# Kernel tuning notes

Hardware: AMD Instinct MI355X
Metric: run time of the kernel (lower is better)

The kernel has to match this reference:

```python
import jax, jax.numpy as jnp
import numpy as np

B, S, D = 2, 2048, 1024
NH, KVH = 16, 4
HD = D // NH  # 64
ROPE_BASE = 10000.0


def rotate_half(x):
    half = x.shape[-1] // 2
    x1, x2 = x[..., :half], x[..., half:]
    return jnp.concatenate((-x2, x1), axis=-1)


def rope_cache(seq_len, head_dim, base, dtype):
    half = head_dim // 2
    inv_freq = 1.0 / (base ** (jnp.arange(half, dtype=jnp.float32) / max(1, half)))
    t = jnp.arange(seq_len, dtype=jnp.float32)
    freqs = jnp.einsum('i,j->ij', t, inv_freq)          # [S, half]
    emb = jnp.concatenate((freqs, freqs), axis=-1)      # [S, HD]
    cos = jnp.cos(emb)[None, None].astype(dtype)        # [1,1,S,HD]
    sin = jnp.sin(emb)[None, None].astype(dtype)
    return sin, cos


def setup_inputs() -> dict:
    key = jax.random.key(0)
    ks = jax.random.split(key, 5)
    s = 0.02
    return {
        'x': jax.random.normal(ks[0], (B, S, D), dtype=jnp.float32),
        'Wq': jax.random.normal(ks[1], (D, D), dtype=jnp.float32) * s,
        'Wk': jax.random.normal(ks[2], (D, KVH * HD), dtype=jnp.float32) * s,
        'Wv': jax.random.normal(ks[3], (D, KVH * HD), dtype=jnp.float32) * s,
        'Wo': jax.random.normal(ks[4], (D, D), dtype=jnp.float32) * s,
    }


def reference(x, Wq, Wk, Wv, Wo):
    bsz, seq_len, _ = x.shape
    scale = HD ** -0.5
    q = (x @ Wq).reshape(bsz, seq_len, NH, HD).transpose(0, 2, 1, 3)   # [B,NH,S,HD]
    k = (x @ Wk).reshape(bsz, seq_len, KVH, HD).transpose(0, 2, 1, 3)  # [B,KVH,S,HD]
    v = (x @ Wv).reshape(bsz, seq_len, KVH, HD).transpose(0, 2, 1, 3)

    sin, cos = rope_cache(seq_len, HD, ROPE_BASE, q.dtype)
    q = q * cos + rotate_half(q) * sin
    k = k * cos + rotate_half(k) * sin

    rep = NH // KVH
    k = jnp.repeat(k, rep, axis=1)  # repeat_interleave over head dim -> [B,NH,S,HD]
    v = jnp.repeat(v, rep, axis=1)

    att = jnp.einsum('bhqd,bhkd->bhqk', q, k) * scale
    causal = jnp.tril(jnp.ones((seq_len, seq_len), dtype=bool))
    att = jnp.where(causal, att, jnp.finfo(att.dtype).min)
    att = jax.nn.softmax(att, axis=-1)

    y = jnp.einsum('bhqk,bhkd->bhqd', att, v)
    y = y.transpose(0, 2, 1, 3).reshape(bsz, seq_len, NH * HD)
    return y @ Wo
```

## Files before the change

### kernel.cpp

```cpp
#include <hip/hip_runtime.h>

typedef __bf16 bf16x8 __attribute__((ext_vector_type(8)));
typedef float  f32x4  __attribute__((ext_vector_type(4)));
typedef float  f32x16 __attribute__((ext_vector_type(16)));
typedef unsigned short u16;
typedef unsigned int u32;
typedef u16 u16x8 __attribute__((ext_vector_type(8)));
typedef u32 u32x4 __attribute__((ext_vector_type(4)));

#define MFMA16(a, b, c) __builtin_amdgcn_mfma_f32_16x16x32_bf16((a), (b), (c), 0, 0, 0)
#define MFMA32(a, b, c) __builtin_amdgcn_mfma_f32_32x32x16_bf16((a), (b), (c), 0, 0, 0)

__device__ __forceinline__ u16 f2bf(float f) {
  __bf16 b = (__bf16)f;
  return __builtin_bit_cast(u16, b);
}
__device__ __forceinline__ bf16x8 ld_bf8(const u16* p) {
  return __builtin_bit_cast(bf16x8, *(const u16x8*)p);
}
__device__ __forceinline__ float ex2(float x) { return __builtin_amdgcn_exp2f(x); }
__device__ __forceinline__ void pswap(u32& a, u32& b) {
  asm("v_permlane32_swap_b32 %0, %1" : "+v"(a), "+v"(b));
}

__global__ __launch_bounds__(256) void k_prep(const float4* __restrict__ x,
                                              ushort4* __restrict__ xb,
                                              const float* __restrict__ Wq,
                                              const float* __restrict__ Wk,
                                              const float* __restrict__ Wv,
                                              const float* __restrict__ Wo,
                                              u16* __restrict__ WqkvT,
                                              u16* __restrict__ WoT,
                                              float2* __restrict__ tab) {
  __shared__ float t[64][65];
  int bid = blockIdx.x;
  if (bid < 4096) {
    int i = bid * 256 + threadIdx.x;
    float4 v = x[i];
    ushort4 o;
    o.x = f2bf(v.x); o.y = f2bf(v.y); o.z = f2bf(v.z); o.w = f2bf(v.w);
    xb[i] = o;
  } else if (bid < 4736) {
    int tb = bid - 4096;
    int n0 = (tb % 40) * 64, k0 = (tb / 40) * 64;
    int c = threadIdx.x & 63, r = threadIdx.x >> 6;
    int n = n0 + c;
    const float* sp; int stride; int nn;
    if (n < 1024)      { sp = Wq; stride = 1024; nn = n; }
    else if (n < 1280) { sp = Wk; stride = 256;  nn = n - 1024; }
    else if (n < 1536) { sp = Wv; stride = 256;  nn = n - 1280; }
    else               { sp = Wo; stride = 1024; nn = n - 1536; }
#pragma unroll
    for (int j = 0; j < 16; ++j)
      t[r + j * 4][c] = sp[(size_t)(k0 + r + j * 4) * stride + nn];
    __syncthreads();
#pragma unroll
    for (int j = 0; j < 16; ++j) {
      int rr = r + j * 4;
      int orow = n0 + rr;
      u16* d = (orow < 1536) ? (WqkvT + (size_t)orow * 1024)
                             : (WoT + (size_t)(orow - 1536) * 1024);
      d[k0 + c] = f2bf(t[c][rr]);
    }
  } else {
    int idx = (bid - 4736) * 256 + threadIdx.x;
    int s = idx >> 5, j = idx & 31;
    const float L2B = 13.287712379549449f / 32.f;
    float ang = (float)s * exp2f(-(float)j * L2B);
    float sn, cs; sincosf(ang, &sn, &cs);
    tab[idx] = make_float2(cs, sn);
  }
}

__global__ __launch_bounds__(256) void k_gemm1(const u16* __restrict__ A,
                                               const u16* __restrict__ Bt,
                                               const float2* __restrict__ tab,
                                               u16* __restrict__ Qa,
                                               u16* __restrict__ Ka,
                                               u16* __restrict__ Vtt) {
  const int K = 1024;
  __shared__ u16 lA[128 * 64];
  __shared__ u16 lB[128 * 64];
  const int t = threadIdx.x;
  const int lane = t & 63;
  const int w = t >> 6;
  const int lg = lane >> 4, lr = lane & 15;
  const int wr = w >> 1, wc = w & 1;
  int f = blockIdx.x;
  int cpx = 384 >> 3;
  int f2 = (f & 7) * cpx + (f >> 3);
  const int n0 = (f2 % 12) * 128, m0 = (f2 / 12) * 128;

  f32x4 acc[4][4];
#pragma unroll
  for (int a = 0; a < 4; ++a)
#pragma unroll
    for (int b = 0; b < 4; ++b) acc[a][b] = (f32x4)0.0f;

  for (int kt = 0; kt < K; kt += 64) {
#pragma unroll
    for (int i = 0; i < 4; ++i) {
      int c = t + i * 256;
      int row = c >> 3, slot = c & 7;
      int k8 = (slot ^ (row & 7)) << 3;
      __builtin_amdgcn_global_load_lds(
          (const __attribute__((address_space(1))) void*)(A + (size_t)(m0 + row) * K + kt + k8),
          (__attribute__((address_space(3))) void*)(&lA[c * 8]), 16, 0, 0);
    }
#pragma unroll
    for (int i = 0; i < 4; ++i) {
      int c = t + i * 256;
      int row = c >> 3, slot = c & 7;
      int k8 = (slot ^ (row & 7)) << 3;
      __builtin_amdgcn_global_load_lds(
          (const __attribute__((address_space(1))) void*)(Bt + (size_t)(n0 + row) * K + kt + k8),
          (__attribute__((address_space(3))) void*)(&lB[c * 8]), 16, 0, 0);
    }
    asm volatile("s_waitcnt vmcnt(0)" ::: "memory");
    __syncthreads();

#pragma unroll
    for (int ks = 0; ks < 2; ++ks) {
      bf16x8 af[4], bff[4];
#pragma unroll
      for (int mf = 0; mf < 4; ++mf) {
        int row = wr * 64 + mf * 16 + lr;
        int eo = (ks * 32 + lg * 8) ^ ((row & 7) << 3);
        af[mf] = ld_bf8(&lA[row * 64 + eo]);
      }
#pragma unroll
      for (int nf = 0; nf < 4; ++nf) {
        int row = wc * 64 + nf * 16 + lr;
        int eo = (ks * 32 + lg * 8) ^ ((row & 7) << 3);
        bff[nf] = ld_bf8(&lB[row * 64 + eo]);
      }
#pragma unroll
      for (int mf = 0; mf < 4; ++mf)
#pragma unroll
        for (int nf = 0; nf < 4; ++nf)
          acc[mf][nf] = MFMA16(af[mf], bff[nf], acc[mf][nf]);
    }
    __syncthreads();
  }

  const int colbase = n0 + wc * 64;
  if (colbase < 1280) {
    const bool isQ = colbase < 1024;
    const float SC = isQ ? 0.18033688f : 1.0f;
    u16* base;
    if (isQ) {
      int hh = colbase >> 6;
      base = Qa + (size_t)hh * 2048 * 64;
    } else {
      int kvh = (colbase - 1024) >> 6;
      base = Ka + (size_t)kvh * 2048 * 64;
    }
    const int hstride = isQ ? 16 : 4;
#pragma unroll
    for (int mf = 0; mf < 4; ++mf)
#pragma unroll
      for (int i2 = 0; i2 < 4; ++i2) {
        int row = m0 + wr * 64 + mf * 16 + lg * 4 + i2;
        int bb = row >> 11, ss = row & 2047;
        float2 t0 = tab[ss * 32 + lr];
        float2 t1 = tab[ss * 32 + 16 + lr];
        float v0 = acc[mf][0][i2], v2 = acc[mf][2][i2];
        float v1 = acc[mf][1][i2], v3 = acc[mf][3][i2];
        u16* dst = base + ((size_t)bb * hstride * 2048 + ss) * 64;
        dst[lr]      = f2bf((v0 * t0.x - v2 * t0.y) * SC);
        dst[lr + 32] = f2bf((v2 * t0.x + v0 * t0.y) * SC);
        dst[lr + 16] = f2bf((v1 * t1.x - v3 * t1.y) * SC);
        dst[lr + 48] = f2bf((v3 * t1.x + v1 * t1.y) * SC);
      }
  } else {
    int kvh = (colbase - 1280) >> 6;
#pragma unroll
    for (int mf = 0; mf < 4; ++mf)
#pragma unroll
      for (int i2 = 0; i2 < 4; ++i2) {
        int row = m0 + wr * 64 + mf * 16 + lg * 4 + i2;
        int bb = row >> 11, ss = row & 2047;
        u16* dst = Vtt + (size_t)(bb * 4 + kvh) * 131072 +
                   (size_t)(ss >> 5) * 2048 + (ss & 31);
#pragma unroll
        for (int nf = 0; nf < 4; ++nf)
          dst[(nf * 16 + lr) * 32] = f2bf(acc[mf][nf][i2]);
      }
  }
}

#define PK2(a, b) ((u32)f2bf(a) | ((u32)f2bf(b) << 16))

#define GLL(SRC, DST) __builtin_amdgcn_global_load_lds(                     \
    (const __attribute__((address_space(1))) void*)(SRC),                   \
    (__attribute__((address_space(3))) void*)(DST), 16, 0, 0)

#define STAGE(DB, J2) do {                                                  \
    GLL(ksrc0 + (size_t)(J2) * 4096,        &kbuf[DB][t * 8]);              \
    GLL(ksrc0 + (size_t)(J2) * 4096 + 2048, &kbuf[DB][2048 + t * 8]);       \
    GLL(vsrc0 + (size_t)(J2) * 4096,        &vbuf[DB][t * 8]);              \
    GLL(vsrc0 + (size_t)(J2) * 4096 + 2048, &vbuf[DB][2048 + t * 8]);       \
  } while (0)

#define SUBC(SOFF, KB, QLIM) do {                                           \
    bf16x8 KF0 = ld_bf8(kb_ + (SOFF) + ql * 64 + (((0 + hi) ^ (ql & 7)) << 3)); \
    bf16x8 KF1 = ld_bf8(kb_ + (SOFF) + ql * 64 + (((2 + hi) ^ (ql & 7)) << 3)); \
    bf16x8 KF2 = ld_bf8(kb_ + (SOFF) + ql * 64 + (((4 + hi) ^ (ql & 7)) << 3)); \
    bf16x8 KF3 = ld_bf8(kb_ + (SOFF) + ql * 64 + (((6 + hi) ^ (ql & 7)) << 3)); \
    bf16x8 VF0 = ld_bf8(vb_ + (SOFF) + ql * 32 + (((0 + hi) ^ (ql & 3)) << 3)); \
    bf16x8 VF1 = ld_bf8(vb_ + (SOFF) + ql * 32 + (((2 + hi) ^ (ql & 3)) << 3)); \
    bf16x8 VF2 = ld_bf8(vb_ + (SOFF) + (32 + ql) * 32 + (((0 + hi) ^ (ql & 3)) << 3)); \
    bf16x8 VF3 = ld_bf8(vb_ + (SOFF) + (32 + ql) * 32 + (((2 + hi) ^ (ql & 3)) << 3)); \
    f32x16 sa_ = MFMA32(KF0, qf0, (f32x16)0.0f);                            \
    sa_ = MFMA32(KF1, qf1, sa_);                                            \
    f32x16 sb_ = MFMA32(KF2, qf2, (f32x16)0.0f);                            \
    sb_ = MFMA32(KF3, qf3, sb_);                                            \
    float p_[16];                                                           \
    _Pragma("unroll")                                                       \
    for (int r = 0; r < 16; ++r) {                                          \
      int kc = (KB) + (r & 3) + 8 * (r >> 2);                               \
      float sv = sa_[r] + sb_[r];                                           \
      p_[r] = (kc > (QLIM)) ? 0.f : ex2(sv);                                \
    }                                                                       \
    { float t0_ = p_[0] + p_[1], t1_ = p_[2] + p_[3];                       \
      float t2_ = p_[4] + p_[5], t3_ = p_[6] + p_[7];                       \
      float t4_ = p_[8] + p_[9], t5_ = p_[10] + p_[11];                     \
      float t6_ = p_[12] + p_[13], t7_ = p_[14] + p_[15];                   \
      lh += ((t0_ + t1_) + (t2_ + t3_)) + ((t4_ + t5_) + (t6_ + t7_)); }    \
    u32 a0 = PK2(p_[0], p_[1]),   a1 = PK2(p_[2], p_[3]);                   \
    u32 a2 = PK2(p_[4], p_[5]),   a3 = PK2(p_[6], p_[7]);                   \
    u32 c0 = PK2(p_[8], p_[9]),   c1 = PK2(p_[10], p_[11]);                 \
    u32 c2 = PK2(p_[12], p_[13]), c3 = PK2(p_[14], p_[15]);                 \
    pswap(a0, a2); pswap(a1, a3); pswap(c0, c2); pswap(c1, c3);             \
    u32x4 w0_, w1_;                                                         \
    w0_.x = a0; w0_.y = a1; w0_.z = a2; w0_.w = a3;                         \
    w1_.x = c0; w1_.y = c1; w1_.z = c2; w1_.w = c3;                         \
    bf16x8 pf0 = __builtin_bit_cast(bf16x8, w0_);                           \
    bf16x8 pf1 = __builtin_bit_cast(bf16x8, w1_);                           \
    o0 = MFMA32(VF0, pf0, o0);                                              \
    o0 = MFMA32(VF1, pf1, o0);                                              \
    o1 = MFMA32(VF2, pf0, o1);                                              \
    o1 = MFMA32(VF3, pf1, o1);                                              \
  } while (0)

__global__ __launch_bounds__(256) void k_attn(const u16* __restrict__ Qa,
                                              const u16* __restrict__ Ka,
                                              const u16* __restrict__ Vtt,
                                              u16* __restrict__ Ob) {
  __shared__ u16 kbuf[2][4096];
  __shared__ u16 vbuf[2][4096];
  const int bid = blockIdx.x;
  const int qb = 15 - (bid >> 5);
  const int bh = bid & 31;
  const int h = bh & 15, b = bh >> 4;
  const int kvh = h >> 2;
  const int t = threadIdx.x;
  const int w = t >> 6;
  const int lane = t & 63;
  const int ql = lane & 31;
  const int hi = lane >> 5;
  const int nt2 = qb * 2 + 2;
  const int jdw = qb * 4 + w;
  const int jd2 = jdw >> 1;
  const int q0w = jdw * 32;
  const int qad = q0w + ql - 4 * hi;

  const u16* Qp = Qa + (size_t)(b * 16 + h) * 2048 * 64;
  const u16* Kp = Ka + (size_t)(b * 4 + kvh) * 2048 * 64;
  const u16* Vp = Vtt + (size_t)(b * 4 + kvh) * 131072;

  const u16* ksrc0 = Kp + (size_t)(t >> 3) * 64 + (((t & 7) ^ ((t >> 3) & 7)) << 3);
  const u16* vsrc0 = Vp + (size_t)(t >> 2) * 32 + (((t & 3) ^ ((t >> 2) & 3)) << 3);

  bf16x8 qf0, qf1, qf2, qf3;
  {
    const u16* qp = Qp + (size_t)(q0w + ql) * 64 + hi * 8;
    qf0 = ld_bf8(qp);      qf1 = ld_bf8(qp + 16);
    qf2 = ld_bf8(qp + 32); qf3 = ld_bf8(qp + 48);
  }

  f32x16 o0 = (f32x16)0.0f, o1 = (f32x16)0.0f;
  float lh = 0.f;

  STAGE(0, 0);
  for (int j2 = 0; j2 < nt2; ++j2) {
    const int cur = j2 & 1;
    if (j2 + 1 < nt2) {
      STAGE(cur ^ 1, j2 + 1);
      asm volatile("s_waitcnt vmcnt(4)" ::: "memory");
    } else {
      asm volatile("s_waitcnt vmcnt(0)" ::: "memory");
    }
    __builtin_amdgcn_s_barrier();
    __builtin_amdgcn_sched_barrier(0);
    const u16* kb_ = kbuf[cur];
    const u16* vb_ = vbuf[cur];
    if (j2 < jd2) {
      SUBC(0, 0, 0x7fffffff);
      SUBC(2048, 0, 0x7fffffff);
    } else if (j2 == jd2) {
      SUBC(0, jd2 * 64, (jdw & 1) ? 0x7fffffff : qad);
      if (jdw & 1) SUBC(2048, jd2 * 64 + 32, qad);
    }
    asm volatile("s_waitcnt lgkmcnt(0)" ::: "memory");
    __builtin_amdgcn_sched_barrier(0);
    __builtin_amdgcn_s_barrier();
  }

  float l = lh + __shfl_xor(lh, 32);
  float li = 1.f / l;
  u16* op = Ob + ((size_t)(b * 2048 + q0w + ql)) * 1024 + h * 64 + hi * 4;
#pragma unroll
  for (int g = 0; g < 4; ++g) {
    ushort4 wv;
    wv.x = f2bf(o0[g * 4 + 0] * li); wv.y = f2bf(o0[g * 4 + 1] * li);
    wv.z = f2bf(o0[g * 4 + 2] * li); wv.w = f2bf(o0[g * 4 + 3] * li);
    *(ushort4*)(op + g * 8) = wv;
    wv.x = f2bf(o1[g * 4 + 0] * li); wv.y = f2bf(o1[g * 4 + 1] * li);
    wv.z = f2bf(o1[g * 4 + 2] * li); wv.w = f2bf(o1[g * 4 + 3] * li);
    *(ushort4*)(op + 32 + g * 8) = wv;
  }
}

__global__ __launch_bounds__(256) void k_gemm2(const u16* __restrict__ A,
                                               const u16* __restrict__ Bt,
                                               float* __restrict__ C) {
  const int K = 1024, N = 1024;
  __shared__ u16 lA[128 * 64];
  __shared__ u16 lB[128 * 64];
  const int t = threadIdx.x;
  const int lane = t & 63;
  const int w = t >> 6;
  const int lg = lane >> 4, lr = lane & 15;
  const int wr = w >> 1, wc = w & 1;
  int f = blockIdx.x;
  int cpx = 256 >> 3;
  int f2 = (f & 7) * cpx + (f >> 3);
  const int n0 = (f2 & 7) * 128, m0 = (f2 >> 3) * 128;

  f32x4 acc[4][4];
#pragma unroll
  for (int a = 0; a < 4; ++a)
#pragma unroll
    for (int b = 0; b < 4; ++b) acc[a][b] = (f32x4)0.0f;

  for (int kt = 0; kt < K; kt += 64) {
#pragma unroll
    for (int i = 0; i < 4; ++i) {
      int c = t + i * 256;
      int row = c >> 3, slot = c & 7;
      int k8 = (slot ^ (row & 7)) << 3;
      __builtin_amdgcn_global_load_lds(
          (const __attribute__((address_space(1))) void*)(A + (size_t)(m0 + row) * K + kt + k8),
          (__attribute__((address_space(3))) void*)(&lA[c * 8]), 16, 0, 0);
    }
#pragma unroll
    for (int i = 0; i < 4; ++i) {
      int c = t + i * 256;
      int row = c >> 3, slot = c & 7;
      int k8 = (slot ^ (row & 7)) << 3;
      __builtin_amdgcn_global_load_lds(
          (const __attribute__((address_space(1))) void*)(Bt + (size_t)(n0 + row) * K + kt + k8),
          (__attribute__((address_space(3))) void*)(&lB[c * 8]), 16, 0, 0);
    }
    asm volatile("s_waitcnt vmcnt(0)" ::: "memory");
    __syncthreads();

#pragma unroll
    for (int ks = 0; ks < 2; ++ks) {
      bf16x8 af[4], bff[4];
#pragma unroll
      for (int mf = 0; mf < 4; ++mf) {
        int row = wr * 64 + mf * 16 + lr;
        int eo = (ks * 32 + lg * 8) ^ ((row & 7) << 3);
        af[mf] = ld_bf8(&lA[row * 64 + eo]);
      }
#pragma unroll
      for (int nf = 0; nf < 4; ++nf) {
        int row = wc * 64 + nf * 16 + lr;
        int eo = (ks * 32 + lg * 8) ^ ((row & 7) << 3);
        bff[nf] = ld_bf8(&lB[row * 64 + eo]);
      }
#pragma unroll
      for (int mf = 0; mf < 4; ++mf)
#pragma unroll
        for (int nf = 0; nf < 4; ++nf)
          acc[mf][nf] = MFMA16(af[mf], bff[nf], acc[mf][nf]);
    }
    __syncthreads();
  }

#pragma unroll
  for (int mf = 0; mf < 4; ++mf)
#pragma unroll
    for (int nf = 0; nf < 4; ++nf) {
      int col = n0 + wc * 64 + nf * 16 + lr;
#pragma unroll
      for (int i = 0; i < 4; ++i) {
        int row = m0 + wr * 64 + mf * 16 + lg * 4 + i;
        C[(size_t)row * N + col] = acc[mf][nf][i];
      }
    }
}

extern "C" void kernel_launch(void* const* d_in, const int* in_sizes, int n_in,
                              void* d_out, int out_size, void* d_ws, size_t ws_size,
                              hipStream_t stream) {
  const float* x  = (const float*)d_in[0];
  const float* Wq = (const float*)d_in[1];
  const float* Wk = (const float*)d_in[2];
  const float* Wv = (const float*)d_in[3];
  const float* Wo = (const float*)d_in[4];
  float* out = (float*)d_out;

  char* ws = (char*)d_ws;
  u16*    xb    = (u16*)(ws);
  u16*    WqkvT = (u16*)(ws + 8388608);
  u16*    WoT   = (u16*)(ws + 11534336);
  float2* tab   = (float2*)(ws + 13631488);
  u16*    Qa    = (u16*)(ws + 14155776);
  u16*    Ka    = (u16*)(ws + 22544384);
  u16*    Vtt   = (u16*)(ws + 26738688);
  u16*    Ob    = (u16*)(ws + 28835840);

  k_prep<<<4992, 256, 0, stream>>>((const float4*)x, (ushort4*)xb, Wq, Wk, Wv, Wo,
                                   WqkvT, WoT, tab);
  k_gemm1<<<384, 256, 0, stream>>>(xb, WqkvT, tab, Qa, Ka, Vtt);
  k_attn<<<512, 256, 0, stream>>>(Qa, Ka, Vtt, Ob);
  k_gemm2<<<256, 256, 0, stream>>>(Ob, WoT, out);
}
```

Baseline: 106.1 us.

## Split KV range of long causal query blocks across two workgroups with reduce

Query blocks 8-15, which carry the longest causal KV ranges, are now split into two workgroups, each covering half of the KV tiles. This grows the grid from 512 to 768 blocks and caps per-block work, to fix tail imbalance. Each half writes an unnormalized partial output in bf16 plus its row-sum. A new reduce kernel adds the two halves and normalizes. The cost is an extra launch, extra global traffic for the partials, and some precision loss from storing unnormalized partials in bf16.

```diff
diff --git a/kernel.cpp b/kernel.cpp
--- a/kernel.cpp
+++ b/kernel.cpp
@@ -14,6 +14,9 @@
 __device__ __forceinline__ u16 f2bf(float f) {
   __bf16 b = (__bf16)f;
   return __builtin_bit_cast(u16, b);
+}
+__device__ __forceinline__ float bf2f(u16 u) {
+  return __builtin_bit_cast(float, (u32)u << 16);
 }
 __device__ __forceinline__ bf16x8 ld_bf8(const u16* p) {
   return __builtin_bit_cast(bf16x8, *(const u16x8*)p);
@@ -246,12 +249,17 @@
 __global__ __launch_bounds__(256) void k_attn(const u16* __restrict__ Qa,
                                               const u16* __restrict__ Ka,
                                               const u16* __restrict__ Vtt,
-                                              u16* __restrict__ Ob) {
+                                              u16* __restrict__ Ob,
+                                              u16* __restrict__ Pb,
+                                              float* __restrict__ Lb) {
   __shared__ u16 kbuf[2][4096];
   __shared__ u16 vbuf[2][4096];
   const int bid = blockIdx.x;
-  const int qb = 15 - (bid >> 5);
   const int bh = bid & 31;
+  const int s = bid >> 5;
+  int qb, half;
+  if (s < 16) { qb = 15 - (s >> 1); half = s & 1; }
+  else        { qb = 23 - s;        half = -1;    }
   const int h = bh & 15, b = bh >> 4;
   const int kvh = h >> 2;
   const int t = threadIdx.x;
@@ -259,11 +267,14 @@
   const int lane = t & 63;
   const int ql = lane & 31;
   const int hi = lane >> 5;
-  const int nt2 = qb * 2 + 2;
   const int jdw = qb * 4 + w;
   const int jd2 = jdw >> 1;
   const int q0w = jdw * 32;
   const int qad = q0w + ql - 4 * hi;
+  int jb2, je2;
+  if (half < 0)       { jb2 = 0;      je2 = 2 * qb + 2; }
+  else if (half == 0) { jb2 = 0;      je2 = qb + 1;     }
+  else                { jb2 = qb + 1; je2 = 2 * qb + 2; }
 
   const u16* Qp = Qa + (size_t)(b * 16 + h) * 2048 * 64;
   const u16* Kp = Ka + (size_t)(b * 4 + kvh) * 2048 * 64;
@@ -282,10 +293,10 @@
   f32x16 o0 = (f32x16)0.0f, o1 = (f32x16)0.0f;
   float lh = 0.f;
 
-  STAGE(0, 0);
-  for (int j2 = 0; j2 < nt2; ++j2) {
-    const int cur = j2 & 1;
-    if (j2 + 1 < nt2) {
+  STAGE(0, jb2);
+  for (int j2 = jb2; j2 < je2; ++j2) {
+    const int cur = (j2 - jb2) & 1;
+    if (j2 + 1 < je2) {
       STAGE(cur ^ 1, j2 + 1);
       asm volatile("s_waitcnt vmcnt(4)" ::: "memory");
     } else {
@@ -295,12 +306,17 @@
     __builtin_amdgcn_sched_barrier(0);
     const u16* kb_ = kbuf[cur];
     const u16* vb_ = vbuf[cur];
-    if (j2 < jd2) {
+    if (half == 0) {
       SUBC(0, 0, 0x7fffffff);
       SUBC(2048, 0, 0x7fffffff);
-    } else if (j2 == jd2) {
-      SUBC(0, jd2 * 64, (jdw & 1) ? 0x7fffffff : qad);
-      if (jdw & 1) SUBC(2048, jd2 * 64 + 32, qad);
+    } else {
+      if (j2 < jd2) {
+        SUBC(0, 0, 0x7fffffff);
+        SUBC(2048, 0, 0x7fffffff);
+      } else if (j2 == jd2) {
+        SUBC(0, jd2 * 64, (jdw & 1) ? 0x7fffffff : qad);
+        if (jdw & 1) SUBC(2048, jd2 * 64 + 32, qad);
+      }
     }
     asm volatile("s_waitcnt lgkmcnt(0)" ::: "memory");
     __builtin_amdgcn_sched_barrier(0);
@@ -308,17 +324,57 @@
   }
 
   float l = lh + __shfl_xor(lh, 32);
-  float li = 1.f / l;
-  u16* op = Ob + ((size_t)(b * 2048 + q0w + ql)) * 1024 + h * 64 + hi * 4;
+  if (half < 0) {
+    float li = 1.f / l;
+    u16* op = Ob + ((size_t)(b * 2048 + q0w + ql)) * 1024 + h * 64 + hi * 4;
+#pragma unroll
+    for (int g = 0; g < 4; ++g) {
+      ushort4 wv;
+      wv.x = f2bf(o0[g * 4 + 0] * li); wv.y = f2bf(o0[g * 4 + 1] * li);
+      wv.z = f2bf(o0[g * 4 + 2] * li); wv.w = f2bf(o0[g * 4 + 3] * li);
+      *(ushort4*)(op + g * 8) = wv;
+      wv.x = f2bf(o1[g * 4 + 0] * li); wv.y = f2bf(o1[g * 4 + 1] * li);
+      wv.z = f2bf(o1[g * 4 + 2] * li); wv.w = f2bf(o1[g * 4 + 3] * li);
+      *(ushort4*)(op + 32 + g * 8) = wv;
+    }
+  } else {
+    const int pslot = (bh * 8 + (qb - 8)) * 2 + half;
+    u16* pp = Pb + ((size_t)pslot * 128 + w * 32 + ql) * 64 + hi * 4;
+#pragma unroll
+    for (int g = 0; g < 4; ++g) {
+      ushort4 wv;
+      wv.x = f2bf(o0[g * 4 + 0]); wv.y = f2bf(o0[g * 4 + 1]);
+      wv.z = f2bf(o0[g * 4 + 2]); wv.w = f2bf(o0[g * 4 + 3]);
+      *(ushort4*)(pp + g * 8) = wv;
+      wv.x = f2bf(o1[g * 4 + 0]); wv.y = f2bf(o1[g * 4 + 1]);
+      wv.z = f2bf(o1[g * 4 + 2]); wv.w = f2bf(o1[g * 4 + 3]);
+      *(ushort4*)(pp + 32 + g * 8) = wv;
+    }
+    if (hi == 0) Lb[pslot * 128 + w * 32 + ql] = l;
+  }
+}
+
+__global__ __launch_bounds__(256) void k_reduce(const u16* __restrict__ Pb,
+                                                const float* __restrict__ Lb,
+                                                u16* __restrict__ Ob) {
+  int bid = blockIdx.x;
+  int bh = bid >> 3, qh = bid & 7;
+  int qb = qh + 8;
+  int h = bh & 15, b = bh >> 4;
+  int pA = (bh * 8 + qh) * 2, pB = pA + 1;
+  int row = threadIdx.x >> 1, dh = (threadIdx.x & 1) * 32;
+  const u16* pa = Pb + ((size_t)pA * 128 + row) * 64 + dh;
+  const u16* pc = Pb + ((size_t)pB * 128 + row) * 64 + dh;
+  float li = 1.f / (Lb[pA * 128 + row] + Lb[pB * 128 + row]);
+  u16* op = Ob + ((size_t)(b * 2048 + qb * 128 + row)) * 1024 + h * 64 + dh;
 #pragma unroll
   for (int g = 0; g < 4; ++g) {
-    ushort4 wv;
-    wv.x = f2bf(o0[g * 4 + 0] * li); wv.y = f2bf(o0[g * 4 + 1] * li);
-    wv.z = f2bf(o0[g * 4 + 2] * li); wv.w = f2bf(o0[g * 4 + 3] * li);
-    *(ushort4*)(op + g * 8) = wv;
-    wv.x = f2bf(o1[g * 4 + 0] * li); wv.y = f2bf(o1[g * 4 + 1] * li);
-    wv.z = f2bf(o1[g * 4 + 2] * li); wv.w = f2bf(o1[g * 4 + 3] * li);
-    *(ushort4*)(op + 32 + g * 8) = wv;
+    u16x8 va = *(const u16x8*)(pa + g * 8);
+    u16x8 vc = *(const u16x8*)(pc + g * 8);
+    u16x8 wv;
+#pragma unroll
+    for (int e = 0; e < 8; ++e) wv[e] = f2bf((bf2f(va[e]) + bf2f(vc[e])) * li);
+    *(u16x8*)(op + g * 8) = wv;
   }
 }
 
@@ -422,10 +478,13 @@
   u16*    Ka    = (u16*)(ws + 22544384);
   u16*    Vtt   = (u16*)(ws + 26738688);
   u16*    Ob    = (u16*)(ws + 28835840);
+  u16*    Pb    = (u16*)(ws + 37224448);
+  float*  Lb    = (float*)(ws + 45613056);
 
   k_prep<<<4992, 256, 0, stream>>>((const float4*)x, (ushort4*)xb, Wq, Wk, Wv, Wo,
                                    WqkvT, WoT, tab);
   k_gemm1<<<384, 256, 0, stream>>>(xb, WqkvT, tab, Qa, Ka, Vtt);
-  k_attn<<<512, 256, 0, stream>>>(Qa, Ka, Vtt, Ob);
+  k_attn<<<768, 256, 0, stream>>>(Qa, Ka, Vtt, Ob, Pb, Lb);
+  k_reduce<<<256, 256, 0, stream>>>(Pb, Lb, Ob);
   k_gemm2<<<256, 256, 0, stream>>>(Ob, WoT, out);
 }
```

After: 106.6 us. Within noise of the previous version (+0.4%).
